# Performance work log

Measured on AMD Instinct MI355X. Metric: run time of the kernel, lower is better.

## Reference

```python
import jax, jax.numpy as jnp
import numpy as np

ALPHA = 0.2          # LeakyReLU negative slope
NEG_FILL = -9e15     # mask value used by the original module


def setup_inputs() -> dict:
    key = jax.random.key(0)
    k1, k2, k3, k4 = jax.random.split(key, 4)
    N, D, H, F = 4096, 512, 8, 64  # nhid*nheads == embedding_dim
    h = jax.random.normal(k1, (N, D), dtype=jnp.float32)
    adj = jax.random.randint(k2, (N, N), 0, 2, dtype=jnp.int32)
    # per-head linear projection weights (no bias) and attention vectors
    W = jax.random.normal(k3, (H, D, F), dtype=jnp.float32) * (1.0 / np.sqrt(D))
    a = jax.random.normal(k4, (H, 2 * F), dtype=jnp.float32) * 0.1
    return {"h": h, "adj": adj, "W": W, "a": a}


def reference(h, adj, W, a):
    H, D, F = W.shape
    N = h.shape[0]
    # per-head projection: [H, N, F]
    hp = jnp.einsum('nd,hdf->hnf', h, W)
    # score(i,j) = leakyrelu(a[:F].h_i + a[F:].h_j)  (decomposed broadcast-add,
    # same math as the original N*N concat construction)
    a_src, a_dst = a[:, :F], a[:, F:]
    f_src = jnp.einsum('hnf,hf->hn', hp, a_src)  # [H, N]
    f_dst = jnp.einsum('hnf,hf->hn', hp, a_dst)  # [H, N]
    e = jax.nn.leaky_relu(f_src[:, :, None] + f_dst[:, None, :], ALPHA)  # [H,N,N]
    e = jnp.where(adj[None] > 0, e, NEG_FILL)
    att = jax.nn.softmax(e, axis=-1)  # softmax over neighbors j (dim=1 in torch)
    out = jnp.einsum('hij,hjf->hif', att, hp)  # [H, N, F]
    # concat heads -> [N, H*F], then ELU
    out = jnp.transpose(out, (1, 0, 2)).reshape(N, H * F)
    return jax.nn.elu(out)
```

## Files before the change

### kernel.cpp

```cpp
#include <hip/hip_runtime.h>

#define NN 4096
#define DD 512
#define HH 8
#define FF 64
#define LRELU_ALPHA 0.2f
#define SP 72
#define JCHUNK 2048

typedef __attribute__((ext_vector_type(8))) short bf16x8;
typedef __attribute__((ext_vector_type(4))) float f32x4;

__device__ __forceinline__ float f4c(const float4& v, int k) {
    return k == 0 ? v.x : (k == 1 ? v.y : (k == 2 ? v.z : v.w));
}
__device__ __forceinline__ void f4s(float4& v, int k, float x) {
    if (k == 0) v.x = x; else if (k == 1) v.y = x; else if (k == 2) v.z = x; else v.w = x;
}
__device__ __forceinline__ unsigned short f2bf(float x) {
    unsigned u = __float_as_uint(x);
    return (unsigned short)((u + 0x7fffu + ((u >> 16) & 1u)) >> 16);
}
__device__ __forceinline__ float bf2f(unsigned short h) {
    return __uint_as_float(((unsigned)h) << 16);
}
__device__ __forceinline__ unsigned fkey(float x) {
    unsigned u = __float_as_uint(x);
    return (u & 0x80000000u) ? ~u : (u | 0x80000000u);
}
__device__ __forceinline__ float funkey(unsigned k) {
    unsigned u = (k & 0x80000000u) ? (k ^ 0x80000000u) : ~k;
    return __uint_as_float(u);
}

__global__ __launch_bounds__(256) void k_prep(const int* __restrict__ adj,
                                              const float* __restrict__ W,
                                              const float* __restrict__ hmat,
                                              unsigned long long* __restrict__ adjm,
                                              unsigned short* __restrict__ wt_hi,
                                              unsigned short* __restrict__ wt_lo,
                                              unsigned short* __restrict__ h_hi,
                                              unsigned short* __restrict__ h_lo,
                                              unsigned* __restrict__ mxkey,
                                              float* __restrict__ hpsum) {
    __shared__ unsigned long long shbuf[2080];
    int b = blockIdx.x, t = threadIdx.x;
    if (b < 2048) {
        int g = b >> 3, cs = b & 7;
        int r0 = g * 16;
        int lane = t & 63, wv = t >> 6;
        unsigned long long (*w64)[9] = (unsigned long long(*)[9])shbuf;
        for (int r = 0; r < 16; r++) {
            #pragma unroll
            for (int q = 0; q < 2; q++) {
                int col = cs * 512 + q * 256 + t;
                unsigned long long m = __ballot(adj[(size_t)(r0 + r) * NN + col] > 0);
                if (lane == 0) w64[r][q * 4 + wv] = m;
            }
        }
        __syncthreads();
        for (int tl = wv; tl < 8; tl += 4) {
            unsigned long long wbits = w64[lane & 15][tl];
            unsigned long long my = 0;
            #pragma unroll
            for (int k = 0; k < 16; k++) {
                int shv = 32 * (k >> 3) + 8 * (lane >> 4) + (k & 7);
                unsigned long long bal = __ballot((unsigned)((wbits >> shv) & 1ULL));
                if (lane == k) my = bal;
            }
            if (lane < 16)
                adjm[((size_t)g * 64 + cs * 8 + tl) * 16 + lane] = my;
        }
    } else if (b < 2112) {
        float (*tile)[65] = (float(*)[65])shbuf;
        int idx = b - 2048;
        int h = idx >> 3;
        int d0 = (idx & 7) * 64;
        #pragma unroll
        for (int kidx = 0; kidx < 4; kidx++) {
            int id = t + 256 * kidx;
            int dd = id >> 4, f4i = (id & 15) * 4;
            float4 v = *(const float4*)(W + ((size_t)(h * DD + d0 + dd)) * FF + f4i);
            tile[dd][f4i] = v.x; tile[dd][f4i + 1] = v.y;
            tile[dd][f4i + 2] = v.z; tile[dd][f4i + 3] = v.w;
        }
        __syncthreads();
        int f = t >> 2, c = (t & 3) * 16;
        union { unsigned short s[16]; uint4 v[2]; } hb, lb;
        #pragma unroll
        for (int q = 0; q < 16; q++) {
            float v = tile[c + q][f];
            unsigned short hi = f2bf(v);
            hb.s[q] = hi;
            lb.s[q] = f2bf(v - bf2f(hi));
        }
        uint4* dh = (uint4*)(wt_hi + ((size_t)h * FF + f) * DD + d0 + c);
        uint4* dl = (uint4*)(wt_lo + ((size_t)h * FF + f) * DD + d0 + c);
        dh[0] = hb.v[0]; dh[1] = hb.v[1];
        dl[0] = lb.v[0]; dl[1] = lb.v[1];
    } else if (b < 2368) {
        int idx = b - 2112;
        int row = idx * 16 + (t >> 4);
        int c0 = (t & 15) * 32;
        const float* src = hmat + (size_t)row * DD + c0;
        #pragma unroll
        for (int half = 0; half < 2; half++) {
            float4 p0 = *(const float4*)(src + half * 16);
            float4 p1 = *(const float4*)(src + half * 16 + 4);
            float4 p2 = *(const float4*)(src + half * 16 + 8);
            float4 p3 = *(const float4*)(src + half * 16 + 12);
            union { unsigned short s[16]; uint4 v[2]; } hb, lb;
            #pragma unroll
            for (int q = 0; q < 16; q++) {
                float v = q < 4 ? f4c(p0, q) : q < 8 ? f4c(p1, q - 4)
                          : q < 12 ? f4c(p2, q - 8) : f4c(p3, q - 12);
                unsigned short hi = f2bf(v);
                hb.s[q] = hi;
                lb.s[q] = f2bf(v - bf2f(hi));
            }
            uint4* dh = (uint4*)(h_hi + (size_t)row * DD + c0 + half * 16);
            uint4* dl = (uint4*)(h_lo + (size_t)row * DD + c0 + half * 16);
            dh[0] = hb.v[0]; dh[1] = hb.v[1];
            dl[0] = lb.v[0]; dl[1] = lb.v[1];
        }
    } else {
        if (t < 16) mxkey[t] = 0u;
        hpsum[t] = 0.f;
        hpsum[t + 256] = 0.f;
    }
}

__global__ __launch_bounds__(256) void k_hp_mfma(const unsigned short* __restrict__ hhi,
                                                 const unsigned short* __restrict__ hlo,
                                                 const unsigned short* __restrict__ whi,
                                                 const unsigned short* __restrict__ wlo,
                                                 const float* __restrict__ a,
                                                 unsigned short* __restrict__ hpT_hi,
                                                 float* __restrict__ fs,
                                                 float* __restrict__ ejs,
                                                 float* __restrict__ fjs,
                                                 float* __restrict__ hpsum,
                                                 unsigned* __restrict__ mxkey) {
    __shared__ char smem[4 * 64 * SP * 2];
    unsigned short* ah = (unsigned short*)smem;
    unsigned short* al = ah + 64 * SP;
    unsigned short* bh = al + 64 * SP;
    unsigned short* bl = bh + 64 * SP;

    int t = threadIdx.x;
    int h = blockIdx.y;
    int n0 = blockIdx.x * 64;
    int lane = t & 63;
    int w = t >> 6;
    int R0 = (w >> 1) * 32, F0 = (w & 1) * 32;
    int am = lane & 15, aq = lane >> 4;
    int sr = t >> 2, sc = (t & 3) * 16;

    const unsigned short* ghh = hhi + (size_t)(n0 + sr) * DD;
    const unsigned short* ghl = hlo + (size_t)(n0 + sr) * DD;
    const unsigned short* gbh = whi + ((size_t)h * FF + sr) * DD;
    const unsigned short* gbl = wlo + ((size_t)h * FF + sr) * DD;

    f32x4 acc[2][2] = {};
    for (int kk = 0; kk < DD; kk += 64) {
        {
            const uint4* s0 = (const uint4*)(ghh + kk + sc);
            const uint4* s1 = (const uint4*)(ghl + kk + sc);
            uint4 h0 = s0[0], h1 = s0[1], l0 = s1[0], l1 = s1[1];
            *(uint4*)(ah + sr * SP + sc) = h0; *(uint4*)(ah + sr * SP + sc + 8) = h1;
            *(uint4*)(al + sr * SP + sc) = l0; *(uint4*)(al + sr * SP + sc + 8) = l1;
        }
        {
            const uint4* s2 = (const uint4*)(gbh + kk + sc);
            const uint4* s3 = (const uint4*)(gbl + kk + sc);
            uint4 w0 = s2[0], w1 = s2[1], x0 = s3[0], x1 = s3[1];
            *(uint4*)(bh + sr * SP + sc) = w0; *(uint4*)(bh + sr * SP + sc + 8) = w1;
            *(uint4*)(bl + sr * SP + sc) = x0; *(uint4*)(bl + sr * SP + sc + 8) = x1;
        }
        __syncthreads();
        #pragma unroll
        for (int k2 = 0; k2 < 2; k2++) {
            int ko = k2 * 32 + aq * 8;
            bf16x8 a0h = *(const bf16x8*)(ah + (R0 + am) * SP + ko);
            bf16x8 a1h = *(const bf16x8*)(ah + (R0 + 16 + am) * SP + ko);
            bf16x8 a0l = *(const bf16x8*)(al + (R0 + am) * SP + ko);
            bf16x8 a1l = *(const bf16x8*)(al + (R0 + 16 + am) * SP + ko);
            bf16x8 b0h = *(const bf16x8*)(bh + (F0 + am) * SP + ko);
            bf16x8 b1h = *(const bf16x8*)(bh + (F0 + 16 + am) * SP + ko);
            bf16x8 b0l = *(const bf16x8*)(bl + (F0 + am) * SP + ko);
            bf16x8 b1l = *(const bf16x8*)(bl + (F0 + 16 + am) * SP + ko);
            acc[0][0] = __builtin_amdgcn_mfma_f32_16x16x32_bf16(a0h, b0h, acc[0][0], 0, 0, 0);
            acc[0][1] = __builtin_amdgcn_mfma_f32_16x16x32_bf16(a0h, b1h, acc[0][1], 0, 0, 0);
            acc[1][0] = __builtin_amdgcn_mfma_f32_16x16x32_bf16(a1h, b0h, acc[1][0], 0, 0, 0);
            acc[1][1] = __builtin_amdgcn_mfma_f32_16x16x32_bf16(a1h, b1h, acc[1][1], 0, 0, 0);
            acc[0][0] = __builtin_amdgcn_mfma_f32_16x16x32_bf16(a0h, b0l, acc[0][0], 0, 0, 0);
            acc[0][1] = __builtin_amdgcn_mfma_f32_16x16x32_bf16(a0h, b1l, acc[0][1], 0, 0, 0);
            acc[1][0] = __builtin_amdgcn_mfma_f32_16x16x32_bf16(a1h, b0l, acc[1][0], 0, 0, 0);
            acc[1][1] = __builtin_amdgcn_mfma_f32_16x16x32_bf16(a1h, b1l, acc[1][1], 0, 0, 0);
            acc[0][0] = __builtin_amdgcn_mfma_f32_16x16x32_bf16(a0l, b0h, acc[0][0], 0, 0, 0);
            acc[0][1] = __builtin_amdgcn_mfma_f32_16x16x32_bf16(a0l, b1h, acc[0][1], 0, 0, 0);
            acc[1][0] = __builtin_amdgcn_mfma_f32_16x16x32_bf16(a1l, b0h, acc[1][0], 0, 0, 0);
            acc[1][1] = __builtin_amdgcn_mfma_f32_16x16x32_bf16(a1l, b1h, acc[1][1], 0, 0, 0);
        }
        __syncthreads();
    }

    unsigned* tt = (unsigned*)smem;
    float* rs = (float*)(smem + 17408);
    float* rd = rs + 256;
    float* ash = rd + 256;
    if (t < 128) ash[t] = a[h * 2 * FF + t];
    int col = lane & 15, rbase = (lane >> 4) * 4;
    #pragma unroll
    for (int m16 = 0; m16 < 2; m16++) {
        #pragma unroll
        for (int n16 = 0; n16 < 2; n16++) {
            #pragma unroll
            for (int r = 0; r < 4; r++) {
                int nl = R0 + m16 * 16 + rbase + r;
                int f = F0 + n16 * 16 + col;
                float v = acc[m16][n16][r];
                unsigned short hi = f2bf(v);
                unsigned short lo = f2bf(v - bf2f(hi));
                tt[f * 68 + nl] = (unsigned)hi | ((unsigned)lo << 16);
            }
        }
    }
    __syncthreads();
    {
        int f = t >> 2, c = (t & 3) * 16;
        union { unsigned short s[16]; uint4 v[2]; } hb;
        float csum = 0.f;
        #pragma unroll
        for (int q = 0; q < 16; q++) {
            unsigned u = tt[f * 68 + c + q];
            hb.s[q] = (unsigned short)(u & 0xffffu);
            csum += bf2f((unsigned short)(u & 0xffffu)) + bf2f((unsigned short)(u >> 16));
        }
        uint4* dh = (uint4*)(hpT_hi + ((size_t)h * FF + f) * NN + n0 + c);
        dh[0] = hb.v[0]; dh[1] = hb.v[1];
        csum += __shfl_xor(csum, 1);
        csum += __shfl_xor(csum, 2);
        if ((t & 3) == 0) unsafeAtomicAdd(hpsum + h * FF + f, csum);
    }
    {
        int n = t & 63, g = t >> 6;
        float fsp = 0.f, fdp = 0.f;
        #pragma unroll
        for (int q = 0; q < 16; q++) {
            int f = g * 16 + q;
            unsigned u = tt[f * 68 + n];
            float v = bf2f((unsigned short)(u & 0xffffu)) + bf2f((unsigned short)(u >> 16));
            fsp += v * ash[f];
            fdp += v * ash[64 + f];
        }
        rs[g * 64 + n] = fsp;
        rd[g * 64 + n] = fdp;
    }
    __syncthreads();
    if (t < 64) {
        const float LOG2E = 1.44269504f;
        float fdv = (rd[t] + rd[64 + t] + rd[128 + t] + rd[192 + t]) * LOG2E;
        fs[(size_t)h * NN + n0 + t] = (rs[t] + rs[64 + t] + rs[128 + t] + rs[192 + t]) * LOG2E;
        ejs[(size_t)h * NN + n0 + t] = __builtin_amdgcn_exp2f(fdv);
        fjs[(size_t)h * NN + n0 + t] = __builtin_amdgcn_exp2f(LRELU_ALPHA * fdv);
        unsigned key = fkey(fdv);
        #pragma unroll
        for (int off = 32; off; off >>= 1) key = max(key, (unsigned)__shfl_xor((int)key, off));
        if (t == 0) atomicMax(mxkey + h, key);
    }
}

__global__ __launch_bounds__(512) void k_attn(const float* __restrict__ fs,
                                              const float* __restrict__ ejs,
                                              const float* __restrict__ fjs,
                                              const unsigned* __restrict__ mxkey,
                                              const unsigned long long* __restrict__ adjm,
                                              const unsigned short* __restrict__ hpT_hi,
                                              const float* __restrict__ hpsum,
                                              float* __restrict__ outp) {
    __shared__ unsigned short hbh[2][2][64 * SP];

    int t = threadIdx.x;
    int h = blockIdx.y;
    int i0 = blockIdx.x * 64;
    int lane = t & 63;
    int w = t >> 6;
    int h2 = w >> 2;
    int rg = w & 3;
    int am = lane & 15, aq = lane >> 4;
    int th = t >> 8;
    int ts = t & 255;
    int sr = ts >> 2, sc = (ts & 3) * 16;

    float mfdL = funkey(mxkey[h]);
    float fsv = fs[(size_t)h * NN + i0 + rg * 16 + am];
    float sL = fsv + mfdL;
    float mrL = fmaxf(sL, LRELU_ALPHA * sL);
    float EA = __builtin_amdgcn_exp2f(fsv - mrL);
    float EC = __builtin_amdgcn_exp2f(LRELU_ALPHA * fsv - mrL);

    int rgu = __builtin_amdgcn_readfirstlane(rg);
    int h2u = __builtin_amdgcn_readfirstlane(h2);
    const unsigned long long* mbase = adjm + ((size_t)(blockIdx.x * 4 + rgu) * 64) * 16;
    const unsigned short* gH = hpT_hi + (size_t)h * FF * NN;
    const float* ejh = ejs + (size_t)h * NN + (size_t)h2u * JCHUNK;
    const float* fjh = fjs + (size_t)h * NN + (size_t)h2u * JCHUNK;

    f32x4 acc[4] = {};
    f32x4 accl = {};
    bf16x8 ones;
    #pragma unroll
    for (int i = 0; i < 8; i++) ones[i] = (short)0x3f80;

    auto stage_load = [&](int j0, uint4& v0, uint4& v1) {
        const uint4* s = (const uint4*)(gH + (size_t)sr * NN + th * JCHUNK + j0 + sc);
        v0 = s[0]; v1 = s[1];
    };
    auto stage_write = [&](int buf, uint4 v0, uint4 v1) {
        *(uint4*)(&hbh[buf][th][sr * SP + sc]) = v0;
        *(uint4*)(&hbh[buf][th][sr * SP + sc + 8]) = v1;
    };
    auto ejf_load = [&](int j0, float4* pe, float4* pf) {
        pe[0] = *(const float4*)(ejh + j0 + aq * 8);
        pe[1] = *(const float4*)(ejh + j0 + aq * 8 + 4);
        pe[2] = *(const float4*)(ejh + j0 + 32 + aq * 8);
        pe[3] = *(const float4*)(ejh + j0 + 32 + aq * 8 + 4);
        pf[0] = *(const float4*)(fjh + j0 + aq * 8);
        pf[1] = *(const float4*)(fjh + j0 + aq * 8 + 4);
        pf[2] = *(const float4*)(fjh + j0 + 32 + aq * 8);
        pf[3] = *(const float4*)(fjh + j0 + 32 + aq * 8 + 4);
    };
    auto mkfrag = [&](const float4* pe, const float4* pf,
                      const unsigned long long* mk, int off) -> bf16x8 {
        unsigned eu[8];
        #pragma unroll
        for (int q = 0; q < 2; q++) {
            float4 ev4 = pe[q], fv4 = pf[q];
            #pragma unroll
            for (int bq = 0; bq < 4; bq++) {
                float e = fmaxf(EA * f4c(ev4, bq), EC * f4c(fv4, bq));
                unsigned r;
                asm("v_cndmask_b32 %0, 0, %1, %2"
                    : "=v"(r) : "v"(e), "s"(mk[off + q * 4 + bq]));
                eu[q * 4 + bq] = r;
            }
        }
        union { unsigned u[4]; bf16x8 v; } pk;
        pk.u[0] = __builtin_amdgcn_perm(eu[1], eu[0], 0x07060302);
        pk.u[1] = __builtin_amdgcn_perm(eu[3], eu[2], 0x07060302);
        pk.u[2] = __builtin_amdgcn_perm(eu[5], eu[4], 0x07060302);
        pk.u[3] = __builtin_amdgcn_perm(eu[7], eu[6], 0x07060302);
        return pk.v;
    };
    auto consume = [&](int cur, bf16x8 P0, bf16x8 P1) {
        #pragma unroll
        for (int k2 = 0; k2 < 2; k2++) {
            int ko = k2 * 32 + aq * 8;
            bf16x8 x0 = *(const bf16x8*)(&hbh[cur][h2][(am)      * SP + ko]);
            bf16x8 x1 = *(const bf16x8*)(&hbh[cur][h2][(am + 16) * SP + ko]);
            bf16x8 x2 = *(const bf16x8*)(&hbh[cur][h2][(am + 32) * SP + ko]);
            bf16x8 x3 = *(const bf16x8*)(&hbh[cur][h2][(am + 48) * SP + ko]);
            bf16x8 P = k2 ? P1 : P0;
            acc[0] = __builtin_amdgcn_mfma_f32_16x16x32_bf16(x0, P, acc[0], 0, 0, 0);
            acc[1] = __builtin_amdgcn_mfma_f32_16x16x32_bf16(x1, P, acc[1], 0, 0, 0);
            acc[2] = __builtin_amdgcn_mfma_f32_16x16x32_bf16(x2, P, acc[2], 0, 0, 0);
            acc[3] = __builtin_amdgcn_mfma_f32_16x16x32_bf16(x3, P, acc[3], 0, 0, 0);
            accl   = __builtin_amdgcn_mfma_f32_16x16x32_bf16(ones, P, accl, 0, 0, 0);
        }
    };

    bf16x8 Pc0, Pc1;
    uint4 svA0, svA1, svB0, svB1;
    float4 peA[4], pfA[4], peB[4], pfB[4];
    unsigned long long mkA[16], mkB[16];

    {
        uint4 v0, v1; float4 pe0[4], pf0[4];
        unsigned long long mk0[16];
        stage_load(0, v0, v1);
        ejf_load(0, pe0, pf0);
        #pragma unroll
        for (int k = 0; k < 16; k++) mk0[k] = mbase[(size_t)(h2u * 32) * 16 + k];
        Pc0 = mkfrag(pe0, pf0, mk0, 0);
        Pc1 = mkfrag(pe0 + 2, pf0 + 2, mk0, 8);
        stage_write(0, v0, v1);
        stage_load(64, svA0, svA1);
        ejf_load(64, peA, pfA);
        #pragma unroll
        for (int k = 0; k < 16; k++) mkA[k] = mbase[(size_t)(h2u * 32 + 1) * 16 + k];
        __syncthreads();
    }

    for (int j0 = 0; j0 < JCHUNK; j0 += 128) {
        {
            stage_write(1, svA0, svA1);
            int j2 = (j0 + 128) & (JCHUNK - 1);
            stage_load(j2, svB0, svB1);
            ejf_load(j2, peB, pfB);
            #pragma unroll
            for (int k = 0; k < 16; k++)
                mkB[k] = mbase[(size_t)(h2u * 32 + (j2 >> 6)) * 16 + k];
            consume(0, Pc0, Pc1);
            Pc0 = mkfrag(peA, pfA, mkA, 0);
            Pc1 = mkfrag(peA + 2, pfA + 2, mkA, 8);
            __syncthreads();
        }
        {
            stage_write(0, svB0, svB1);
            int j3 = (j0 + 192) & (JCHUNK - 1);
            stage_load(j3, svA0, svA1);
            ejf_load(j3, peA, pfA);
            #pragma unroll
            for (int k = 0; k < 16; k++)
                mkA[k] = mbase[(size_t)(h2u * 32 + (j3 >> 6)) * 16 + k];
            consume(1, Pc0, Pc1);
            Pc0 = mkfrag(peB, pfB, mkB, 0);
            Pc1 = mkfrag(peB + 2, pfB + 2, mkB, 8);
            __syncthreads();
        }
    }

    float* cb = (float*)hbh;
    if (h2 == 1) {
        #pragma unroll
        for (int mf = 0; mf < 4; mf++)
            *(f32x4*)&cb[((rg * 4 + mf) * 64 + lane) * 4] = acc[mf];
        cb[4096 + rg * 64 + lane] = accl[0];
    }
    __syncthreads();
    if (h2 == 0) {
        #pragma unroll
        for (int mf = 0; mf < 4; mf++) {
            f32x4 o = *(const f32x4*)&cb[((rg * 4 + mf) * 64 + lane) * 4];
            acc[mf] += o;
        }
        float li = accl[0] + cb[4096 + rg * 64 + lane];
        const float invN = 1.0f / NN;
        float rl = 1.f / li;
        int row = i0 + rg * 16 + am;
        float* orow = outp + (size_t)row * (HH * FF) + h * FF;
        #pragma unroll
        for (int mf = 0; mf < 4; mf++) {
            float4 ov;
            #pragma unroll
            for (int r = 0; r < 4; r++) {
                int f = mf * 16 + aq * 4 + r;
                float v;
                if (li > 0.f) v = acc[mf][r] * rl;
                else          v = hpsum[h * FF + f] * invN;
                v = v > 0.f ? v : __expf(v) - 1.f;
                f4s(ov, r, v);
            }
            *(float4*)(orow + mf * 16 + aq * 4) = ov;
        }
    }
}

extern "C" void kernel_launch(void* const* d_in, const int* in_sizes, int n_in,
                              void* d_out, int out_size, void* d_ws, size_t ws_size,
                              hipStream_t stream) {
    const float* hmat = (const float*)d_in[0];
    const int*   adj  = (const int*)d_in[1];
    const float* W    = (const float*)d_in[2];
    const float* a    = (const float*)d_in[3];
    float* out = (float*)d_out;

    char* ws = (char*)d_ws;
    unsigned short* hpT_hi = (unsigned short*)(ws);
    unsigned long long* adjm = (unsigned long long*)(ws + (4u << 20));
    unsigned short* wt_hi  = (unsigned short*)(ws + (6u << 20));
    unsigned short* wt_lo  = (unsigned short*)(ws + (6u << 20) + (512u << 10));
    float* fs    = (float*)(ws + (7u << 20));
    float* ejs   = (float*)(ws + (7u << 20) + (128u << 10));
    unsigned* mxkey = (unsigned*)(ws + (7u << 20) + (256u << 10));
    float* hpsum = (float*)(mxkey + 16);
    float* fjs   = (float*)(ws + (7u << 20) + (384u << 10));
    unsigned short* h_hi = (unsigned short*)(ws + (8u << 20));
    unsigned short* h_lo = (unsigned short*)(ws + (12u << 20));

    k_prep   <<<dim3(2369),          256, 0, stream>>>(adj, W, hmat, adjm, wt_hi, wt_lo,
                                                       h_hi, h_lo, mxkey, hpsum);
    k_hp_mfma<<<dim3(64, 8),         256, 0, stream>>>(h_hi, h_lo, wt_hi, wt_lo, a,
                                                       hpT_hi, fs, ejs, fjs, hpsum, mxkey);
    k_attn   <<<dim3(NN / 64, HH),   512, 0, stream>>>(fs, ejs, fjs, mxkey, adjm,
                                                       hpT_hi, hpsum, out);
}
```

Baseline: 191.7 us.

## Simplify main loop to single-step prefetch instead of two-deep register pipeline

Replaces the unrolled two-stage loop, which kept two sets of prefetched tiles, score vectors and masks in registers (A/B), with a plain loop of step 64. Each iteration prefetches only the next chunk, runs the MFMAs on the current LDS buffer, then writes the next buffer and builds the next P fragments. This cuts live registers, which may raise occupancy or remove spills. The cost is less latency hiding, since global loads now have only one MFMA block in which to land before they are consumed.

```diff
diff --git a/kernel.cpp b/kernel.cpp
--- a/kernel.cpp
+++ b/kernel.cpp
@@ -353,7 +353,31 @@
         pk.u[3] = __builtin_amdgcn_perm(eu[7], eu[6], 0x07060302);
         return pk.v;
     };
-    auto consume = [&](int cur, bf16x8 P0, bf16x8 P1) {
+
+    bf16x8 Pc0, Pc1;
+    {
+        uint4 v0, v1; float4 pe[4], pf[4];
+        stage_load(0, v0, v1);
+        ejf_load(0, pe, pf);
+        unsigned long long mk[16];
+        #pragma unroll
+        for (int k = 0; k < 16; k++) mk[k] = mbase[(size_t)(h2u * 32) * 16 + k];
+        Pc0 = mkfrag(pe, pf, mk, 0);
+        Pc1 = mkfrag(pe + 2, pf + 2, mk, 8);
+        stage_write(0, v0, v1);
+        __syncthreads();
+    }
+
+    for (int j0 = 0; j0 < JCHUNK; j0 += 64) {
+        int cur = (j0 >> 6) & 1;
+        int jn = (j0 + 64) & (JCHUNK - 1);
+        uint4 v0, v1; float4 pe[4], pf[4];
+        stage_load(jn, v0, v1);
+        ejf_load(jn, pe, pf);
+        unsigned long long mk[16];
+        #pragma unroll
+        for (int k = 0; k < 16; k++) mk[k] = mbase[(size_t)(h2u * 32 + (jn >> 6)) * 16 + k];
+
         #pragma unroll
         for (int k2 = 0; k2 < 2; k2++) {
             int ko = k2 * 32 + aq * 8;
@@ -361,64 +385,18 @@
             bf16x8 x1 = *(const bf16x8*)(&hbh[cur][h2][(am + 16) * SP + ko]);
             bf16x8 x2 = *(const bf16x8*)(&hbh[cur][h2][(am + 32) * SP + ko]);
             bf16x8 x3 = *(const bf16x8*)(&hbh[cur][h2][(am + 48) * SP + ko]);
-            bf16x8 P = k2 ? P1 : P0;
+            bf16x8 P = k2 ? Pc1 : Pc0;
             acc[0] = __builtin_amdgcn_mfma_f32_16x16x32_bf16(x0, P, acc[0], 0, 0, 0);
             acc[1] = __builtin_amdgcn_mfma_f32_16x16x32_bf16(x1, P, acc[1], 0, 0, 0);
             acc[2] = __builtin_amdgcn_mfma_f32_16x16x32_bf16(x2, P, acc[2], 0, 0, 0);
             acc[3] = __builtin_amdgcn_mfma_f32_16x16x32_bf16(x3, P, acc[3], 0, 0, 0);
             accl   = __builtin_amdgcn_mfma_f32_16x16x32_bf16(ones, P, accl, 0, 0, 0);
         }
-    };
-
-    bf16x8 Pc0, Pc1;
-    uint4 svA0, svA1, svB0, svB1;
-    float4 peA[4], pfA[4], peB[4], pfB[4];
-    unsigned long long mkA[16], mkB[16];
-
-    {
-        uint4 v0, v1; float4 pe0[4], pf0[4];
-        unsigned long long mk0[16];
-        stage_load(0, v0, v1);
-        ejf_load(0, pe0, pf0);
-        #pragma unroll
-        for (int k = 0; k < 16; k++) mk0[k] = mbase[(size_t)(h2u * 32) * 16 + k];
-        Pc0 = mkfrag(pe0, pf0, mk0, 0);
-        Pc1 = mkfrag(pe0 + 2, pf0 + 2, mk0, 8);
-        stage_write(0, v0, v1);
-        stage_load(64, svA0, svA1);
-        ejf_load(64, peA, pfA);
-        #pragma unroll
-        for (int k = 0; k < 16; k++) mkA[k] = mbase[(size_t)(h2u * 32 + 1) * 16 + k];
-        __syncthreads();
-    }
-
-    for (int j0 = 0; j0 < JCHUNK; j0 += 128) {
-        {
-            stage_write(1, svA0, svA1);
-            int j2 = (j0 + 128) & (JCHUNK - 1);
-            stage_load(j2, svB0, svB1);
-            ejf_load(j2, peB, pfB);
-            #pragma unroll
-            for (int k = 0; k < 16; k++)
-                mkB[k] = mbase[(size_t)(h2u * 32 + (j2 >> 6)) * 16 + k];
-            consume(0, Pc0, Pc1);
-            Pc0 = mkfrag(peA, pfA, mkA, 0);
-            Pc1 = mkfrag(peA + 2, pfA + 2, mkA, 8);
-            __syncthreads();
-        }
-        {
-            stage_write(0, svB0, svB1);
-            int j3 = (j0 + 192) & (JCHUNK - 1);
-            stage_load(j3, svA0, svA1);
-            ejf_load(j3, peA, pfA);
-            #pragma unroll
-            for (int k = 0; k < 16; k++)
-                mkA[k] = mbase[(size_t)(h2u * 32 + (j3 >> 6)) * 16 + k];
-            consume(1, Pc0, Pc1);
-            Pc0 = mkfrag(peB, pfB, mkB, 0);
-            Pc1 = mkfrag(peB + 2, pfB + 2, mkB, 8);
-            __syncthreads();
-        }
+
+        stage_write(cur ^ 1, v0, v1);
+        Pc0 = mkfrag(pe, pf, mk, 0);
+        Pc1 = mkfrag(pe + 2, pf + 2, mk, 8);
+        __syncthreads();
     }
 
     float* cb = (float*)hbh;
```

Measured after the change: 191.1 us. No clear change (-0.3%).
